# Optimization experiments

Hardware: AMD Instinct MI355X
Metric: run time of the kernel (lower is better)

The kernel has to match this reference:

```python
import jax, jax.numpy as jnp
import numpy as np

B, N_WALLS, N_PARAMS = 2048, 32, 6
INF = jnp.float32(1e9)


def _dist(v):
    # Euclidean norm over last axis
    return jnp.sqrt(jnp.sum(jnp.square(v), axis=-1))


def _side_ratio(a, b):
    smaller = jnp.minimum(a, b)
    bigger = jnp.maximum(a, b)
    safe = jnp.where(bigger > 0.0, bigger, 1.0)
    return jnp.where(bigger > 0.0, smaller / safe, 0.0)


def _bounding_box(start, end, dif, width):
    per = jnp.stack([dif[..., 1], -dif[..., 0]], axis=-1)
    per_dist = _dist(per)[..., None]
    per = jnp.where(per_dist > 0.0, per / jnp.where(per_dist > 0.0, per_dist, 1.0), per)
    per = per * width[..., None] / 2.0
    corners = jnp.stack([start + per, start - per, end + per, end - per], axis=-2)
    right = jnp.max(corners[..., 0], axis=-1)
    top = jnp.max(corners[..., 1], axis=-1)
    center = (start + end) / 2.0
    bb_w = jnp.abs((right - center[..., 0]) * 2.0)
    bb_h = jnp.abs((top - center[..., 1]) * 2.0)
    return bb_w * bb_h, bb_w, bb_h


def _param_distance(pt, pp):
    start_t, start_p = pt[..., :2], pp[..., :2]
    end_t, end_p = pt[..., 2:4], pp[..., 2:4]
    width_t, width_p = pt[..., 4], pp[..., 4]
    dif_t, dif_p = end_t - start_t, end_p - start_p
    center_t, center_p = (start_t + end_t) / 2.0, (start_p + end_p) / 2.0
    len_t, len_p = _dist(dif_t), _dist(dif_p)
    center_d = jnp.square(_dist(center_t - center_p))
    area_t, area_p = len_t * width_t, len_p * width_p
    area_d = jnp.square(area_t - area_p)
    lwr_d = jnp.square(_side_ratio(width_t, len_t) - _side_ratio(width_p, len_p))
    bba_t, bbx_t, bby_t = _bounding_box(start_t, end_t, dif_t, width_t)
    bba_p, bbx_p, bby_p = _bounding_box(start_p, end_p, dif_p, width_p)
    ar_t = jnp.where(bba_t > 0.001, area_t / jnp.where(bba_t > 0.001, bba_t, 1.0), 1.0)
    ar_p = jnp.where(bba_p > 0.001, area_p / jnp.where(bba_p > 0.001, bba_p, 1.0), 1.0)
    rot_d = jnp.square(ar_t - ar_p)
    horiz_d = jnp.square(jnp.abs(bbx_t - bbx_p))
    vert_d = jnp.square(jnp.abs(bby_t - bby_p))
    return area_d + center_d + rot_d + horiz_d + vert_d + lwr_d


def _distance_function(true_mx, pred_mx):
    probs_t = true_mx[..., -1]
    probs_p = pred_mx[..., -1]
    prob_d = jnp.square(probs_t - probs_p)
    param_d = _param_distance(true_mx[..., :-1], pred_mx[..., :-1])
    return 10.0 * prob_d + param_d * probs_t


def _hungarian(cost):
    # Exact minimal-cost assignment (shortest augmenting path / JV), vmapped over batch.
    n = cost.shape[-1]
    rows = jnp.arange(n)

    def solve(c):
        def outer(i0, carry):
            u, v, col4row, row4col = carry
            init = (jnp.int32(i0), jnp.zeros(n, bool), jnp.zeros(n, bool),
                    jnp.full(n, INF), jnp.full(n, -1, jnp.int32),
                    jnp.float32(0.0), jnp.int32(-1))

            def cond(s):
                return s[6] < 0

            def body(s):
                i, SR, SC, spc, path, minVal, sink = s
                SR = SR.at[i].set(True)
                slack = minVal + c[i] - u[i] - v
                better = (~SC) & (slack < spc)
                spc = jnp.where(better, slack, spc)
                path = jnp.where(better, i, path)
                masked = jnp.where(SC, INF, spc)
                j = jnp.argmin(masked).astype(jnp.int32)
                minVal = masked[j]
                SC = SC.at[j].set(True)
                r = row4col[j]
                sink = jnp.where(r < 0, j, jnp.int32(-1))
                return (r, SR, SC, spc, path, minVal, sink)

            _, SR, SC, spc, path, minVal, sink = jax.lax.while_loop(cond, body, init)
            u = u + jnp.where(SR & (rows != i0), minVal - spc[col4row], 0.0)
            u = u.at[i0].add(minVal)
            v = v - jnp.where(SC, minVal - spc, 0.0)

            def aug_cond(s):
                return ~s[3]

            def aug_body(s):
                j, c4r, r4c, _ = s
                i = path[j]
                r4c = r4c.at[j].set(i)
                j_next = c4r[i]
                c4r = c4r.at[i].set(j)
                return (j_next, c4r, r4c, i == i0)

            _, col4row, row4col, _ = jax.lax.while_loop(
                aug_cond, aug_body, (sink, col4row, row4col, False))
            return (u, v, col4row, row4col)

        u, v, col4row, row4col = jax.lax.fori_loop(
            0, n, outer,
            (jnp.zeros(n), jnp.zeros(n), jnp.full(n, -1, jnp.int32), jnp.full(n, -1, jnp.int32)))
        return jnp.zeros((n, n), bool).at[rows, col4row].set(True)

    return jax.vmap(solve)(cost)


def setup_inputs() -> dict:
    key = jax.random.key(0)
    k1, k2 = jax.random.split(key)
    params_true = jax.random.uniform(k1, (B, N_WALLS, N_PARAMS), dtype=jnp.float32)
    params_pred = jax.random.uniform(k2, (B, N_WALLS, N_PARAMS), dtype=jnp.float32)
    return {"params_true": params_true, "params_pred": params_pred}


def reference(params_true, params_pred):
    # pairwise set distance: true varies over axis 1, pred over axis 2
    pred_mx = jnp.broadcast_to(params_pred[:, None, :, :], (B, N_WALLS, N_WALLS, N_PARAMS))
    true_mx = jnp.broadcast_to(params_true[:, :, None, :], (B, N_WALLS, N_WALLS, N_PARAMS))
    edges = _distance_function(true_mx, pred_mx)          # [B, N, N]
    pairing = _hungarian(edges)                           # bool [B, N, N]
    loss = jnp.sum(jnp.where(pairing, edges, 0.0), axis=(1, 2))  # [B]
    return loss
```

## Files before the change

kernel.cpp:

```cpp
#include <hip/hip_runtime.h>

#define NW 32
#define BATCH 2048
#define BIGF 1e9f

template <int CTRL>
__device__ __forceinline__ unsigned dpp_umin_step(unsigned x) {
    unsigned t = (unsigned)__builtin_amdgcn_update_dpp((int)x, (int)x, CTRL, 0xF, 0xF, false);
    return t < x ? t : x;
}

__device__ __forceinline__ unsigned wave_umin32_key(unsigned red) {
    red = dpp_umin_step<0x111>(red);
    red = dpp_umin_step<0x112>(red);
    red = dpp_umin_step<0x114>(red);
    red = dpp_umin_step<0x118>(red);
    unsigned kA = (unsigned)__builtin_amdgcn_readlane((int)red, 15);
    unsigned kB = (unsigned)__builtin_amdgcn_readlane((int)red, 31);
    return kA < kB ? kA : kB;
}

__device__ __forceinline__ float readlane_f(float v, int lane) {
    return __int_as_float(__builtin_amdgcn_readlane(__float_as_int(v), lane));
}

__global__ __launch_bounds__(64) void floorplan_hungarian_kernel(
    const float* __restrict__ params_true,
    const float* __restrict__ params_pred,
    float* __restrict__ out)
{
    const int b    = blockIdx.x;
    const int lane = threadIdx.x;

    __shared__ float cost[NW][NW + 1];
    __shared__ float featT[NW][9];
    __shared__ float featP[NW][9];
    __shared__ int   rw[NW];

    {
        const float* src = (lane < NW)
            ? (params_true + ((size_t)b * NW + lane) * 6)
            : (params_pred + ((size_t)b * NW + (lane - NW)) * 6);
        float sx = src[0], sy = src[1], ex = src[2], ey = src[3];
        float w  = src[4], prob = src[5];

        float dx = ex - sx, dy = ey - sy;
        float cx = (sx + ex) * 0.5f, cy = (sy + ey) * 0.5f;
        float len = sqrtf(dx * dx + dy * dy);
        float area = len * w;

        float smaller = fminf(w, len), bigger = fmaxf(w, len);
        float sr = (bigger > 0.0f) ? (smaller / bigger) : 0.0f;

        float px = dy, py = -dx;
        float pd = len;
        if (pd > 0.0f) { px /= pd; py /= pd; }
        px *= w * 0.5f; py *= w * 0.5f;
        float right = fmaxf(fmaxf(sx + px, sx - px), fmaxf(ex + px, ex - px));
        float top   = fmaxf(fmaxf(sy + py, sy - py), fmaxf(ey + py, ey - py));
        float bbw = fabsf((right - cx) * 2.0f);
        float bbh = fabsf((top   - cy) * 2.0f);
        float bba = bbw * bbh;
        float ar  = (bba > 0.001f) ? (area / bba) : 1.0f;

        float* f = (lane < NW) ? featT[lane] : featP[lane - NW];
        f[0] = cx;  f[1] = cy;  f[2] = area; f[3] = sr;
        f[4] = ar;  f[5] = bbw; f[6] = bbh;  f[7] = prob;
    }
    if (lane < NW) rw[lane] = 64;
    __syncthreads();

    float cmin = BIGF; int cargmin = 0;
    for (int e = lane; e < NW * NW; e += 64) {
        int i = e >> 5, j = e & 31;
        float dcx = featT[i][0] - featP[j][0];
        float dcy = featT[i][1] - featP[j][1];
        float center_d = dcx * dcx + dcy * dcy;
        float da = featT[i][2] - featP[j][2];   float area_d  = da * da;
        float ds = featT[i][3] - featP[j][3];   float lwr_d   = ds * ds;
        float dr = featT[i][4] - featP[j][4];   float rot_d   = dr * dr;
        float dxw = featT[i][5] - featP[j][5];  float horiz_d = dxw * dxw;
        float dyh = featT[i][6] - featP[j][6];  float vert_d  = dyh * dyh;
        float probt = featT[i][7], probp = featP[j][7];
        float dp = probt - probp;               float prob_d  = dp * dp;
        float param_d = area_d + center_d + rot_d + horiz_d + vert_d + lwr_d;
        float val = 10.0f * prob_d + param_d * probt;
        cost[i][j] = val;
        if (val < cmin) { cmin = val; cargmin = i; }
    }
    {
        float om = __shfl_xor(cmin, 32);
        int   oi = __shfl_xor(cargmin, 32);
        if (om < cmin || (om == cmin && oi < cargmin)) { cmin = om; cargmin = oi; }
    }
    __syncthreads();

    if (lane < NW) atomicMin(&rw[cargmin], lane);
    __syncthreads();

    const bool isCol = lane < NW;
    const int  col   = lane & 31;
    float v_col   = isCol ? cmin : 0.0f;
    float u_row   = 0.0f;
    int   win     = isCol ? rw[lane] : 64;
    int   col4row = (isCol && win < 64) ? win : -1;
    int   row4col = (isCol && rw[cargmin] == lane) ? cargmin : -1;
    __syncthreads();

    unsigned rem      = (unsigned)(__ballot(isCol && col4row < 0) & 0xffffffffull);
    unsigned freeCols = (unsigned)(__ballot(isCol && row4col < 0) & 0xffffffffull);

    {
        unsigned g = rem;
        while (g != 0) {
            int i = __ffs(g) - 1;
            g &= (g - 1);
            float cij = cost[i][col];
            float slack = cij - v_col;
            unsigned key = isCol
                ? ((__float_as_uint(slack) & 0xFFFFFFE0u) | (unsigned)col)
                : 0xFFFFFFFFu;
            unsigned kmin = wave_umin32_key(key);
            int   j1 = (int)(kmin & 31u);
            float m1 = __uint_as_float(kmin & 0xFFFFFFE0u);
            if (lane == i) u_row = m1;
            if ((freeCols >> j1) & 1u) {
                if (lane == j1) row4col = i;
                if (lane == i)  col4row = j1;
                freeCols &= ~(1u << j1);
                rem      &= ~(1u << i);
            }
        }
    }

    {
        while (rem != 0) {
            int i0 = __ffs(rem) - 1;
            rem &= (rem - 1);

            bool     SCb     = !isCol;
            unsigned spcKey  = 0xFFFFFFFFu;
            int      pathReg = 0;
            unsigned srMask  = 1u << i0;
            float    minValF = 0.0f;
            int      i = i0;
            int      sink;

            float cij = cost[i][col];
            while (true) {
                float u_i = readlane_f(u_row, i);
                float t   = (minValF - v_col) - u_i;
                float slack = fmaxf(t + cij, 0.0f);
                unsigned key = (__float_as_uint(slack) & 0xFFFFFFE0u) | (unsigned)col;
                unsigned old = spcKey;
                unsigned mn  = key < spcKey ? key : spcKey;
                spcKey = SCb ? spcKey : mn;
                pathReg = (spcKey != old) ? i : pathReg;
                unsigned red = SCb ? 0xFFFFFFFFu : spcKey;

                unsigned kmin = wave_umin32_key(red);
                int j = (int)(kmin & 31u);
                minValF = __uint_as_float(kmin & 0xFFFFFFE0u);
                SCb = SCb || (lane == j);
                int r = __builtin_amdgcn_readlane(row4col, j);
                if ((freeCols >> j) & 1u) { sink = j; break; }
                i = r;
                srMask |= (1u << i);
                cij = cost[i][col];
            }

            {
                float spcF = __uint_as_float(spcKey & 0xFFFFFFE0u);
                int gidx = (col4row < 0) ? 0 : col4row;
                float spc_at_c4r = __shfl(spcF, gidx);
                bool in_SR = isCol && ((srMask >> col) & 1u);
                if (lane == i0)              u_row += minValF;
                else if (in_SR)              u_row += minValF - spc_at_c4r;
                if (isCol && SCb)            v_col -= (minValF - spcF);
            }

            {
                int j = sink;
                freeCols &= ~(1u << sink);
                while (true) {
                    int ii = __builtin_amdgcn_readlane(pathReg, j);
                    if (lane == j) row4col = ii;
                    int j_next = __builtin_amdgcn_readlane(col4row, ii);
                    if (lane == ii) col4row = j;
                    if (ii == i0) break;
                    j = j_next;
                }
            }
        }
    }

    float myedge = (isCol && col4row >= 0) ? cost[lane][col4row] : 0.0f;
    #pragma unroll
    for (int off = 32; off >= 1; off >>= 1)
        myedge += __shfl_xor(myedge, off);
    if (lane == 0) out[b] = myedge;
}

extern "C" void kernel_launch(void* const* d_in, const int* in_sizes, int n_in,
                              void* d_out, int out_size, void* d_ws, size_t ws_size,
                              hipStream_t stream) {
    const float* params_true = (const float*)d_in[0];
    const float* params_pred = (const float*)d_in[1];
    float* out = (float*)d_out;
    floorplan_hungarian_kernel<<<BATCH, 64, 0, stream>>>(params_true, params_pred, out);
}
```

Measured before the change: 114.0 us.

## Replace greedy init with augmenting row reduction using second-minimum slack

The initial assignment phase now performs a Jonker-Volgenant style augmenting row reduction. For each unassigned row it finds the lowest and second-lowest reduced costs. It raises the row dual by the second minimum and lowers the column dual by the gap, then may steal an assigned column and requeue the displaced row. The goal is to leave fewer unassigned rows for the costly shortest-augmenting-path loop. In exchange each step does an extra wave reduction, and a guard counter caps the iterations.

Result: slower. 153.6 us (+34.7%).

```diff
diff --git a/kernel.cpp b/kernel.cpp
--- a/kernel.cpp
+++ b/kernel.cpp
@@ -111,26 +111,43 @@
     unsigned freeCols = (unsigned)(__ballot(isCol && row4col < 0) & 0xffffffffull);
 
     {
-        unsigned g = rem;
-        while (g != 0) {
-            int i = __ffs(g) - 1;
-            g &= (g - 1);
+        unsigned q = rem;
+        rem = 0u;
+        int guard = 128;
+        while (q != 0 && guard-- > 0) {
+            int i = __ffs(q) - 1;
+            q &= (q - 1);
+            float u_i = readlane_f(u_row, i);
             float cij = cost[i][col];
-            float slack = cij - v_col;
+            float slack = fmaxf(cij - u_i - v_col, 0.0f);
             unsigned key = isCol
                 ? ((__float_as_uint(slack) & 0xFFFFFFE0u) | (unsigned)col)
                 : 0xFFFFFFFFu;
-            unsigned kmin = wave_umin32_key(key);
-            int   j1 = (int)(kmin & 31u);
-            float m1 = __uint_as_float(kmin & 0xFFFFFFE0u);
-            if (lane == i) u_row = m1;
-            if ((freeCols >> j1) & 1u) {
-                if (lane == j1) row4col = i;
+            unsigned k1  = wave_umin32_key(key);
+            int      j1  = (int)(k1 & 31u);
+            unsigned m1q = k1 & 0xFFFFFFE0u;
+            unsigned key2 = (col == j1) ? 0xFFFFFFFFu : key;
+            unsigned k2  = wave_umin32_key(key2);
+            unsigned m2q = k2 & 0xFFFFFFE0u;
+            float m1f = __uint_as_float(m1q);
+            float m2f = __uint_as_float(m2q);
+            if (lane == i) u_row += m2f;
+            int  kprev  = __builtin_amdgcn_readlane(row4col, j1);
+            bool j1free = (freeCols >> j1) & 1u;
+            if (j1free || m1q < m2q) {
+                if (lane == j1) { v_col -= (m2f - m1f); row4col = i; }
                 if (lane == i)  col4row = j1;
-                freeCols &= ~(1u << j1);
-                rem      &= ~(1u << i);
+                if (j1free) {
+                    freeCols &= ~(1u << j1);
+                } else {
+                    if (lane == kprev) col4row = -1;
+                    q |= (1u << kprev);
+                }
+            } else {
+                rem |= (1u << i);
             }
         }
+        rem |= q;
     }
 
     {
```

## Grow shortest augmenting paths from all free rows at once in Hungarian solver

Applied to the files above, without the earlier changes.

Rewrites the augmenting phase so each Dijkstra search is seeded from every unassigned row at the same time, in place of a single source row. Only one augmentation happens per search, and the path is traced back until it reaches a row with no assigned column, which is then removed from the remaining set. All source rows get their duals raised by the final minimum. This aims to make searches shorter, so fewer serial wave reductions run per augmentation. It changes the dual-update logic, which risks correctness and tie-break differences against the reference.

Result: slower. 123.9 us (+8.6%).

```diff
diff --git a/kernel.cpp b/kernel.cpp
--- a/kernel.cpp
+++ b/kernel.cpp
@@ -135,38 +135,48 @@
 
     {
         while (rem != 0) {
-            int i0 = __ffs(rem) - 1;
-            rem &= (rem - 1);
-
+            const unsigned srcs = rem;
             bool     SCb     = !isCol;
             unsigned spcKey  = 0xFFFFFFFFu;
             int      pathReg = 0;
-            unsigned srMask  = 1u << i0;
+            unsigned srMask  = srcs;
             float    minValF = 0.0f;
-            int      i = i0;
             int      sink;
 
-            float cij = cost[i][col];
+            {
+                unsigned s = srcs;
+                while (s != 0) {
+                    int i = __ffs(s) - 1;
+                    s &= (s - 1);
+                    float u_i = readlane_f(u_row, i);
+                    float cij = cost[i][col];
+                    float sl  = fmaxf(cij - u_i - v_col, 0.0f);
+                    unsigned key = (__float_as_uint(sl) & 0xFFFFFFE0u) | (unsigned)col;
+                    unsigned old = spcKey;
+                    unsigned mn  = key < spcKey ? key : spcKey;
+                    spcKey = SCb ? spcKey : mn;
+                    pathReg = (spcKey != old) ? i : pathReg;
+                }
+            }
+
             while (true) {
-                float u_i = readlane_f(u_row, i);
-                float t   = (minValF - v_col) - u_i;
-                float slack = fmaxf(t + cij, 0.0f);
-                unsigned key = (__float_as_uint(slack) & 0xFFFFFFE0u) | (unsigned)col;
-                unsigned old = spcKey;
-                unsigned mn  = key < spcKey ? key : spcKey;
-                spcKey = SCb ? spcKey : mn;
-                pathReg = (spcKey != old) ? i : pathReg;
                 unsigned red = SCb ? 0xFFFFFFFFu : spcKey;
-
                 unsigned kmin = wave_umin32_key(red);
                 int j = (int)(kmin & 31u);
                 minValF = __uint_as_float(kmin & 0xFFFFFFE0u);
                 SCb = SCb || (lane == j);
                 int r = __builtin_amdgcn_readlane(row4col, j);
                 if ((freeCols >> j) & 1u) { sink = j; break; }
-                i = r;
-                srMask |= (1u << i);
-                cij = cost[i][col];
+                srMask |= (1u << r);
+                float u_i = readlane_f(u_row, r);
+                float cij = cost[r][col];
+                float t   = (minValF - v_col) - u_i;
+                float sl  = fmaxf(t + cij, 0.0f);
+                unsigned key = (__float_as_uint(sl) & 0xFFFFFFE0u) | (unsigned)col;
+                unsigned old = spcKey;
+                unsigned mn  = key < spcKey ? key : spcKey;
+                spcKey = SCb ? spcKey : mn;
+                pathReg = (spcKey != old) ? r : pathReg;
             }
 
             {
@@ -174,7 +184,8 @@
                 int gidx = (col4row < 0) ? 0 : col4row;
                 float spc_at_c4r = __shfl(spcF, gidx);
                 bool in_SR = isCol && ((srMask >> col) & 1u);
-                if (lane == i0)              u_row += minValF;
+                bool isSrc = isCol && ((srcs   >> col) & 1u);
+                if (isSrc)                   u_row += minValF;
                 else if (in_SR)              u_row += minValF - spc_at_c4r;
                 if (isCol && SCb)            v_col -= (minValF - spcF);
             }
@@ -184,11 +195,11 @@
                 freeCols &= ~(1u << sink);
                 while (true) {
                     int ii = __builtin_amdgcn_readlane(pathReg, j);
-                    if (lane == j) row4col = ii;
-                    int j_next = __builtin_amdgcn_readlane(col4row, ii);
+                    int jn = __builtin_amdgcn_readlane(col4row, ii);
+                    if (lane == j)  row4col = ii;
                     if (lane == ii) col4row = j;
-                    if (ii == i0) break;
-                    j = j_next;
+                    if (jn < 0) { rem &= ~(1u << ii); break; }
+                    j = jn;
                 }
             }
         }
```
